# Kernel optimization log

Hardware: AMD Instinct MI355X
Metric: run time of the kernel (lower is better)

Reference implementation:

```python
import jax, jax.numpy as jnp
import numpy as np

NUM_HEADS = 8
CHUNK = 64


def setup_inputs() -> dict:
    key = jax.random.key(0)
    k1, k2, k3, k4 = jax.random.split(key, 4)
    B, C, H, W = 16, 384, 64, 64
    x = jax.random.normal(k1, (B, C, H, W), dtype=jnp.float32)
    # torch nn.Linear weights are [out, in]; qkv has no bias (qkv_bias=False)
    qkv_w = jax.random.normal(k2, (3 * C, C), dtype=jnp.float32) * (C ** -0.5)
    proj_w = jax.random.normal(k3, (C, C), dtype=jnp.float32) * (C ** -0.5)
    proj_b = jax.random.normal(k4, (C,), dtype=jnp.float32) * 0.02
    return {"x": x, "qkv_w": qkv_w, "proj_w": proj_w, "proj_b": proj_b}


def reference(x, qkv_w, proj_w, proj_b):
    B, C, H, W = x.shape
    N = H * W
    nh = NUM_HEADS
    hd = C // nh
    scale = hd ** -0.5
    nc = N // CHUNK  # number of non-overlapping local blocks

    t = x.reshape(B, C, N).transpose(0, 2, 1)  # [B, N, C]
    qkv = t @ qkv_w.T  # [B, N, 3C]
    qkv = qkv.reshape(B, N, 3, nh, hd).transpose(2, 0, 3, 1, 4)  # [3, B, nh, N, hd]
    q, k, v = qkv[0], qkv[1], qkv[2]

    # block-local attention: reshape N -> (nc, CHUNK) and batch over blocks
    q = q.reshape(B, nh, nc, CHUNK, hd)
    k = k.reshape(B, nh, nc, CHUNK, hd)
    v = v.reshape(B, nh, nc, CHUNK, hd)

    scores = jnp.einsum('bhnqd,bhnkd->bhnqk', q, k) * scale  # [B,nh,nc,CHUNK,CHUNK]
    attn = jax.nn.softmax(scores, axis=-1)
    out = jnp.einsum('bhnqk,bhnkd->bhnqd', attn, v)  # [B,nh,nc,CHUNK,hd]

    out = out.reshape(B, nh, N, hd).transpose(0, 2, 1, 3).reshape(B, N, C)
    out = out @ proj_w.T + proj_b
    return out.transpose(0, 2, 1).reshape(B, C, H, W)
```

## Files before the change

### kernel.cpp

```cpp
#include <hip/hip_runtime.h>
#include <stdint.h>

#define NH 8
#define HD 48
#define CC 384
#define NN 4096
#define CK 384

typedef short short8 __attribute__((ext_vector_type(8)));
typedef float floatx4 __attribute__((ext_vector_type(4)));

__device__ inline unsigned short f32_to_bf16_bits(float f) {
    uint32_t u = __builtin_bit_cast(uint32_t, f);
    u = (u + 0x7FFFu + ((u >> 16) & 1u)) >> 16;
    return (unsigned short)u;
}
__device__ inline short8 load8(const unsigned short* p) {
    return *reinterpret_cast<const short8*>(p);
}
typedef __attribute__((address_space(1))) const void gvoid_t;
typedef __attribute__((address_space(3))) void lvoid_t;
__device__ inline void async16(const unsigned short* g, unsigned short* l) {
    __builtin_amdgcn_global_load_lds((gvoid_t*)g, (lvoid_t*)l, 16, 0, 0);
}

__global__ __launch_bounds__(256) void k_cvt(
    const float* __restrict__ src, unsigned short* __restrict__ dst, int n8)
{
    int i = blockIdx.x * 256 + threadIdx.x;
    if (i >= n8) return;
    const float* s = src + (size_t)i * 8;
    unsigned short t[8];
    #pragma unroll
    for (int j = 0; j < 8; ++j) t[j] = f32_to_bf16_bits(s[j]);
    *reinterpret_cast<short8*>(dst + (size_t)i * 8) = *reinterpret_cast<short8*>(t);
}

__global__ __launch_bounds__(256) void k_tr(
    const float* __restrict__ x, unsigned short* __restrict__ xT)
{
    __shared__ unsigned short tile[64][72];
    int bx = blockIdx.x;
    int nt = bx & 63; int rest = bx >> 6; int ct = rest % 6; int b = rest / 6;
    int c0 = ct * 64, n0 = nt * 64;
    int t = threadIdx.x;
    int nl = t & 63, w = t >> 6;
    const float* xb = x + (size_t)b * CC * NN;
    #pragma unroll
    for (int i = 0; i < 4; ++i) {
        int cl = w * 16 + i * 4;
        unsigned short u[4];
        #pragma unroll
        for (int j = 0; j < 4; ++j)
            u[j] = f32_to_bf16_bits(xb[(size_t)(c0 + cl + j) * NN + n0 + nl]);
        *reinterpret_cast<uint2*>(&tile[nl][cl]) = *reinterpret_cast<uint2*>(u);
    }
    __syncthreads();
    #pragma unroll
    for (int it = 0; it < 2; ++it) {
        int v = it * 256 + t;
        int row = v >> 3, seg = v & 7;
        *reinterpret_cast<short8*>(xT + ((size_t)b * NN + n0 + row) * CK + c0 + seg * 8) =
            load8(&tile[row][seg * 8]);
    }
}

__global__ __launch_bounds__(256) void k_qkv(
    const unsigned short* __restrict__ A,
    const unsigned short* __restrict__ W,
    unsigned short* __restrict__ QK,
    unsigned short* __restrict__ Vt)
{
    __shared__ unsigned short smem[17408];
    unsigned short* As = smem;
    unsigned short* Ws = smem + 8192;
    int bx = blockIdx.x;
    int tf = bx % 9, tm = bx / 9;
    int m0 = tm * 128, f0 = tf * 128;
    int tid = threadIdx.x, wid = tid >> 6, lane = tid & 63;
    int l15 = lane & 15, quad = lane >> 4;
    int wm = wid & 1, wn = wid >> 1;

    const unsigned short* Ab = A + (size_t)m0 * CK;
    const unsigned short* Wb = W + (size_t)f0 * CK;

    floatx4 acc[4][4] = {};

    for (int kk = 0; kk < 6; ++kk) {
        int k0 = kk * 64;
        #pragma unroll
        for (int i = 0; i < 4; ++i) {
            int c = i * 256 + tid;
            async16(Ab + (size_t)(c >> 3) * CK + k0 + (c & 7) * 8, As + (i * 256 + wid * 64) * 8);
            async16(Wb + (size_t)(c >> 3) * CK + k0 + (c & 7) * 8, Ws + (i * 256 + wid * 64) * 8);
        }
        __syncthreads();
        #pragma unroll
        for (int ks = 0; ks < 2; ++ks) {
            short8 a[4], bf[4];
            #pragma unroll
            for (int i = 0; i < 4; ++i)
                a[i] = load8(As + (wm * 64 + i * 16 + l15) * 64 + ks * 32 + quad * 8);
            #pragma unroll
            for (int j = 0; j < 4; ++j)
                bf[j] = load8(Ws + (wn * 64 + j * 16 + l15) * 64 + ks * 32 + quad * 8);
            #pragma unroll
            for (int i = 0; i < 4; ++i)
                #pragma unroll
                for (int j = 0; j < 4; ++j)
                    acc[i][j] = __builtin_amdgcn_mfma_f32_16x16x32_bf16(a[i], bf[j], acc[i][j], 0, 0, 0);
        }
        __syncthreads();
    }

    int b = m0 >> 12, nb = m0 & 4095;
    if (tf < 6) {
        #pragma unroll
        for (int i = 0; i < 4; ++i)
            #pragma unroll
            for (int j = 0; j < 4; ++j)
                #pragma unroll
                for (int r = 0; r < 4; ++r)
                    smem[(wm * 64 + i * 16 + quad * 4 + r) * 128 + wn * 64 + j * 16 + l15] =
                        f32_to_bf16_bits(acc[i][j][r]);
        __syncthreads();
        #pragma unroll
        for (int it = 0; it < 8; ++it) {
            int c = it * 256 + tid;
            int row = c >> 4, seg = c & 15;
            *reinterpret_cast<short8*>(QK + (size_t)(m0 + row) * 768 + f0 + seg * 8) =
                load8(smem + row * 128 + seg * 8);
        }
    } else {
        #pragma unroll
        for (int i = 0; i < 4; ++i)
            #pragma unroll
            for (int j = 0; j < 4; ++j)
                #pragma unroll
                for (int r = 0; r < 4; ++r)
                    smem[(wn * 64 + j * 16 + l15) * 136 + wm * 64 + i * 16 + quad * 4 + r] =
                        f32_to_bf16_bits(acc[i][j][r]);
        __syncthreads();
        int fvb = (tf - 6) * 128;
        #pragma unroll
        for (int it = 0; it < 8; ++it) {
            int c = it * 256 + tid;
            int fl = c >> 4, seg = c & 15;
            int fv = fvb + fl;
            int h = fv / 48, d = fv - h * 48;
            *reinterpret_cast<short8*>(Vt + (((size_t)(b * 8 + h) * 48 + d) << 12) + nb + seg * 8) =
                load8(smem + fl * 136 + seg * 8);
        }
    }
}

__global__ __launch_bounds__(256) void k_attn(
    const unsigned short* __restrict__ QK,
    const unsigned short* __restrict__ Vt,
    unsigned short* __restrict__ AO)
{
    __shared__ unsigned short ql[64][64];
    __shared__ unsigned short kl[64][64];
    __shared__ unsigned short vt[48][72];
    __shared__ float          sc[64][66];
    __shared__ unsigned short pl[64][72];

    int bx = blockIdx.x;
    int cn = bx & 63, h = (bx >> 6) & 7, b = bx >> 9;
    int n0 = cn * 64;
    int tid = threadIdx.x, wid = tid >> 6, lane = tid & 63;
    int l15 = lane & 15, quad = lane >> 4;
    int m0w = wid * 16;
    int h48 = h * 48;
    size_t b4 = (size_t)b * NN + n0;

    for (int v = tid; v < 768; v += 256) {
        int mat = v / 384;
        int idx = v - mat * 384;
        int rr = idx / 6, seg = idx - rr * 6;
        uint4 val = *reinterpret_cast<const uint4*>(QK + (b4 + rr) * 768 + mat * 384 + h48 + seg * 8);
        unsigned short* dst = mat ? &kl[rr][seg * 8] : &ql[rr][seg * 8];
        *reinterpret_cast<uint4*>(dst) = val;
    }
    {
        short8 z = {};
        int v = tid;
        if (v < 256) {
            int mat = v >> 7, rr = (v >> 1) & 63, half = v & 1;
            unsigned short* dst = mat ? &kl[rr][48 + half * 8] : &ql[rr][48 + half * 8];
            *reinterpret_cast<short8*>(dst) = z;
        }
    }
    for (int v = tid; v < 384; v += 256) {
        int d = v >> 3, seg = v & 7;
        *reinterpret_cast<uint4*>(&vt[d][seg * 8]) =
            *reinterpret_cast<const uint4*>(Vt + (((size_t)(b * 8 + h) * 48 + d) << 12) + n0 + seg * 8);
    }
    __syncthreads();

    const float scale = 0.14433756729740643f;
    #pragma unroll
    for (int t = 0; t < 4; ++t) {
        floatx4 sacc = {};
        #pragma unroll
        for (int ks = 0; ks < 2; ++ks) {
            short8 a  = load8(&ql[m0w + l15][ks * 32 + quad * 8]);
            short8 bb = load8(&kl[t * 16 + l15][ks * 32 + quad * 8]);
            sacc = __builtin_amdgcn_mfma_f32_16x16x32_bf16(a, bb, sacc, 0, 0, 0);
        }
        #pragma unroll
        for (int r = 0; r < 4; ++r)
            sc[m0w + quad * 4 + r][t * 16 + l15] = sacc[r] * scale;
    }
    __syncthreads();

    {
        int row = m0w + l15;
        int jb  = quad * 16;
        float ev[16];
        #pragma unroll
        for (int jj = 0; jj < 16; ++jj) ev[jj] = sc[row][jb + jj];
        float m = ev[0];
        #pragma unroll
        for (int jj = 1; jj < 16; ++jj) m = fmaxf(m, ev[jj]);
        m = fmaxf(m, __shfl_xor(m, 16));
        m = fmaxf(m, __shfl_xor(m, 32));
        float s = 0.f;
        #pragma unroll
        for (int jj = 0; jj < 16; ++jj) { ev[jj] = __expf(ev[jj] - m); s += ev[jj]; }
        s += __shfl_xor(s, 16);
        s += __shfl_xor(s, 32);
        float inv = 1.0f / s;
        #pragma unroll
        for (int jj = 0; jj < 16; ++jj) pl[row][jb + jj] = f32_to_bf16_bits(ev[jj] * inv);
    }
    __syncthreads();

    #pragma unroll
    for (int t = 0; t < 3; ++t) {
        floatx4 oacc = {};
        #pragma unroll
        for (int ks = 0; ks < 2; ++ks) {
            short8 a  = load8(&pl[m0w + l15][ks * 32 + quad * 8]);
            short8 bb = load8(&vt[t * 16 + l15][ks * 32 + quad * 8]);
            oacc = __builtin_amdgcn_mfma_f32_16x16x32_bf16(a, bb, oacc, 0, 0, 0);
        }
        #pragma unroll
        for (int r = 0; r < 4; ++r)
            kl[m0w + quad * 4 + r][t * 16 + l15] = f32_to_bf16_bits(oacc[r]);
    }
    __syncthreads();

    for (int v = tid; v < 384; v += 256) {
        int rr = v / 6, seg = v - rr * 6;
        *reinterpret_cast<short8*>(AO + (b4 + rr) * CC + h48 + seg * 8) =
            load8(&kl[rr][seg * 8]);
    }
}

__global__ __launch_bounds__(256) void k_proj(
    const unsigned short* __restrict__ A,
    const unsigned short* __restrict__ W,
    const float* __restrict__ bias,
    float* __restrict__ out)
{
    __shared__ unsigned short smem[17408];
    unsigned short* As = smem;
    unsigned short* Ws = smem + 8192;
    float* fs = (float*)smem;
    int bx = blockIdx.x;
    int tf = bx % 3, tm = bx / 3;
    int m0 = tm * 128, f0 = tf * 128;
    int tid = threadIdx.x, wid = tid >> 6, lane = tid & 63;
    int l15 = lane & 15, quad = lane >> 4;
    int wm = wid & 1, wn = wid >> 1;

    const unsigned short* Ab = A + (size_t)m0 * CK;
    const unsigned short* Wb = W + (size_t)f0 * CK;

    floatx4 acc[4][4] = {};

    for (int kk = 0; kk < 6; ++kk) {
        int k0 = kk * 64;
        #pragma unroll
        for (int i = 0; i < 4; ++i) {
            int c = i * 256 + tid;
            async16(Ab + (size_t)(c >> 3) * CK + k0 + (c & 7) * 8, As + (i * 256 + wid * 64) * 8);
            async16(Wb + (size_t)(c >> 3) * CK + k0 + (c & 7) * 8, Ws + (i * 256 + wid * 64) * 8);
        }
        __syncthreads();
        #pragma unroll
        for (int ks = 0; ks < 2; ++ks) {
            short8 a[4], bf[4];
            #pragma unroll
            for (int i = 0; i < 4; ++i)
                a[i] = load8(As + (wm * 64 + i * 16 + l15) * 64 + ks * 32 + quad * 8);
            #pragma unroll
            for (int j = 0; j < 4; ++j)
                bf[j] = load8(Ws + (wn * 64 + j * 16 + l15) * 64 + ks * 32 + quad * 8);
            #pragma unroll
            for (int i = 0; i < 4; ++i)
                #pragma unroll
                for (int j = 0; j < 4; ++j)
                    acc[i][j] = __builtin_amdgcn_mfma_f32_16x16x32_bf16(a[i], bf[j], acc[i][j], 0, 0, 0);
        }
        __syncthreads();
    }

    int b = m0 >> 12, nb = m0 & 4095;
    #pragma unroll
    for (int hh = 0; hh < 2; ++hh) {
        if (wn == hh) {
            #pragma unroll
            for (int j = 0; j < 4; ++j) {
                float bv = bias[f0 + hh * 64 + j * 16 + l15];
                #pragma unroll
                for (int i = 0; i < 4; ++i)
                    #pragma unroll
                    for (int r = 0; r < 4; ++r)
                        fs[(j * 16 + l15) * 132 + wm * 64 + i * 16 + quad * 4 + r] =
                            acc[i][j][r] + bv;
            }
        }
        __syncthreads();
        #pragma unroll
        for (int it = 0; it < 8; ++it) {
            int c = it * 256 + tid;
            int cl = c >> 5, seg = c & 31;
            *reinterpret_cast<float4*>(
                out + (((size_t)(b * CC + f0 + hh * 64 + cl)) << 12) + nb + seg * 4) =
                *reinterpret_cast<const float4*>(fs + cl * 132 + seg * 4);
        }
        __syncthreads();
    }
}

extern "C" void kernel_launch(void* const* d_in, const int* in_sizes, int n_in,
                              void* d_out, int out_size, void* d_ws, size_t ws_size,
                              hipStream_t stream) {
    const float* x      = (const float*)d_in[0];
    const float* qkv_w  = (const float*)d_in[1];
    const float* proj_w = (const float*)d_in[2];
    const float* proj_b = (const float*)d_in[3];
    float* out = (float*)d_out;

    const size_t nX  = (size_t)16 * CC * NN;
    const size_t nW1 = (size_t)3 * CC * CC;
    const size_t nW2 = (size_t)CC * CC;

    unsigned short* xT  = (unsigned short*)d_ws;
    unsigned short* w1b = xT  + nX;
    unsigned short* w2b = w1b + nW1;
    unsigned short* QK  = w2b + nW2;
    unsigned short* Vt  = QK  + (size_t)16 * NN * 768;
    unsigned short* AO  = Vt  + (size_t)16 * 8 * 48 * NN;

    k_tr  <<<dim3(16 * 6 * 64), dim3(256), 0, stream>>>(x, xT);
    k_cvt <<<dim3((int)(nW1 / 8 + 255) / 256), dim3(256), 0, stream>>>(qkv_w, w1b, (int)(nW1 / 8));
    k_cvt <<<dim3((int)(nW2 / 8 + 255) / 256), dim3(256), 0, stream>>>(proj_w, w2b, (int)(nW2 / 8));

    k_qkv <<<dim3(512 * 9), dim3(256), 0, stream>>>(xT, w1b, QK, Vt);
    k_attn<<<dim3(16 * 8 * 64), dim3(256), 0, stream>>>(QK, Vt, AO);
    k_proj<<<dim3(512 * 3), dim3(256), 0, stream>>>(AO, w2b, proj_b, out);
}
```

Measured before the change: 393.1 us.

## Fuse block attention with output projection and remap QKV blocks per XCD

Merges the attention and projection kernels into one kernel per 64-token chunk. The kernel loops over all 8 heads, keeps the attention output for the chunk in LDS, then multiplies it by the projection weights read directly from global memory. This removes the AO round trip through global memory and one launch. The softmax now stays in registers and is redistributed to the PV matmul with shuffles instead of going through LDS. The QKV GEMM block index is also remapped so that consecutive row tiles land on the same XCD for L2 locality. The risks are a large LDS footprint that lowers occupancy, only 1024 blocks, and weights loaded from global without LDS staging.

Measured after the change: 487.2 us. 23.9% more time.

```diff
diff --git a/kernel.cpp b/kernel.cpp
--- a/kernel.cpp
+++ b/kernel.cpp
@@ -75,7 +75,9 @@
     unsigned short* As = smem;
     unsigned short* Ws = smem + 8192;
     int bx = blockIdx.x;
-    int tf = bx % 9, tm = bx / 9;
+    int xcd = bx & 7, idx = bx >> 3;
+    int tm = xcd * 64 + idx / 9;
+    int tf = idx % 9;
     int m0 = tm * 128, f0 = tf * 128;
     int tid = threadIdx.x, wid = tid >> 6, lane = tid & 63;
     int l15 = lane & 15, quad = lane >> 4;
@@ -154,184 +156,145 @@
     }
 }
 
-__global__ __launch_bounds__(256) void k_attn(
+__global__ __launch_bounds__(256) void k_ap(
     const unsigned short* __restrict__ QK,
     const unsigned short* __restrict__ Vt,
-    unsigned short* __restrict__ AO)
+    const unsigned short* __restrict__ W2,
+    const float* __restrict__ bias,
+    float* __restrict__ out)
 {
-    __shared__ unsigned short ql[64][64];
-    __shared__ unsigned short kl[64][64];
+    __shared__ unsigned short kl[64][56];
     __shared__ unsigned short vt[48][72];
-    __shared__ float          sc[64][66];
-    __shared__ unsigned short pl[64][72];
+    __shared__ unsigned short ao[64][392];
 
     int bx = blockIdx.x;
-    int cn = bx & 63, h = (bx >> 6) & 7, b = bx >> 9;
+    int cn = bx & 63, b = bx >> 6;
     int n0 = cn * 64;
     int tid = threadIdx.x, wid = tid >> 6, lane = tid & 63;
     int l15 = lane & 15, quad = lane >> 4;
-    int m0w = wid * 16;
-    int h48 = h * 48;
-    size_t b4 = (size_t)b * NN + n0;
-
-    for (int v = tid; v < 768; v += 256) {
-        int mat = v / 384;
-        int idx = v - mat * 384;
-        int rr = idx / 6, seg = idx - rr * 6;
-        uint4 val = *reinterpret_cast<const uint4*>(QK + (b4 + rr) * 768 + mat * 384 + h48 + seg * 8);
-        unsigned short* dst = mat ? &kl[rr][seg * 8] : &ql[rr][seg * 8];
-        *reinterpret_cast<uint4*>(dst) = val;
-    }
-    {
-        short8 z = {};
-        int v = tid;
-        if (v < 256) {
-            int mat = v >> 7, rr = (v >> 1) & 63, half = v & 1;
-            unsigned short* dst = mat ? &kl[rr][48 + half * 8] : &ql[rr][48 + half * 8];
-            *reinterpret_cast<short8*>(dst) = z;
-        }
-    }
-    for (int v = tid; v < 384; v += 256) {
-        int d = v >> 3, seg = v & 7;
-        *reinterpret_cast<uint4*>(&vt[d][seg * 8]) =
-            *reinterpret_cast<const uint4*>(Vt + (((size_t)(b * 8 + h) * 48 + d) << 12) + n0 + seg * 8);
+    bool hi = quad >= 2;
+    size_t rowbase = (size_t)b * NN + n0;
+
+    const float scale = 0.14433756729740643f;
+    const unsigned short* qrow = QK + (rowbase + wid * 16 + l15) * 768;
+    int d1 = 32 + ((quad & 1) << 3);
+    short8 z8 = {};
+
+    for (int h = 0; h < 8; ++h) {
+        int h48 = h * 48;
+        __syncthreads();
+        for (int v = tid; v < 384; v += 256) {
+            int r = v / 6, sg = v - r * 6;
+            *reinterpret_cast<uint4*>(&kl[r][sg * 8]) =
+                *reinterpret_cast<const uint4*>(QK + (rowbase + r) * 768 + 384 + h48 + sg * 8);
+        }
+        const unsigned short* vbase = Vt + (((size_t)(b * 8 + h) * 48) << 12) + n0;
+        for (int v = tid; v < 384; v += 256) {
+            int d = v >> 3, sg = v & 7;
+            *reinterpret_cast<uint4*>(&vt[d][sg * 8]) =
+                *reinterpret_cast<const uint4*>(vbase + ((size_t)d << 12) + sg * 8);
+        }
+        __syncthreads();
+
+        short8 qf0 = load8(qrow + h48 + quad * 8);
+        short8 qf1 = load8(qrow + h48 + d1);
+        if (hi) qf1 = z8;
+
+        floatx4 st[4];
+        #pragma unroll
+        for (int tk = 0; tk < 4; ++tk) {
+            floatx4 s = {};
+            short8 ka = load8(&kl[tk * 16 + l15][quad * 8]);
+            s = __builtin_amdgcn_mfma_f32_16x16x32_bf16(ka, qf0, s, 0, 0, 0);
+            short8 kb = load8(&kl[tk * 16 + l15][d1]);
+            if (hi) kb = z8;
+            s = __builtin_amdgcn_mfma_f32_16x16x32_bf16(kb, qf1, s, 0, 0, 0);
+            st[tk] = s;
+        }
+
+        float mx = -1e30f;
+        #pragma unroll
+        for (int tk = 0; tk < 4; ++tk)
+            #pragma unroll
+            for (int r = 0; r < 4; ++r) {
+                st[tk][r] *= scale;
+                mx = fmaxf(mx, st[tk][r]);
+            }
+        mx = fmaxf(mx, __shfl_xor(mx, 16));
+        mx = fmaxf(mx, __shfl_xor(mx, 32));
+        float sum = 0.f;
+        #pragma unroll
+        for (int tk = 0; tk < 4; ++tk)
+            #pragma unroll
+            for (int r = 0; r < 4; ++r) {
+                st[tk][r] = __expf(st[tk][r] - mx);
+                sum += st[tk][r];
+            }
+        sum += __shfl_xor(sum, 16);
+        sum += __shfl_xor(sum, 32);
+        float inv = 1.0f / sum;
+        #pragma unroll
+        for (int tk = 0; tk < 4; ++tk)
+            #pragma unroll
+            for (int r = 0; r < 4; ++r)
+                st[tk][r] *= inv;
+
+        int idxA = ((quad & 1) << 5) + l15;
+        int idxB = idxA + 16;
+        short8 pfrag[2];
+        #pragma unroll
+        for (int ks = 0; ks < 2; ++ks) {
+            unsigned short pb[8];
+            #pragma unroll
+            for (int r = 0; r < 4; ++r) {
+                float a0 = __shfl(st[2 * ks + 0][r], idxA);
+                float a1 = __shfl(st[2 * ks + 1][r], idxA);
+                pb[r] = f32_to_bf16_bits(hi ? a1 : a0);
+                float b0 = __shfl(st[2 * ks + 0][r], idxB);
+                float b1 = __shfl(st[2 * ks + 1][r], idxB);
+                pb[4 + r] = f32_to_bf16_bits(hi ? b1 : b0);
+            }
+            pfrag[ks] = *reinterpret_cast<short8*>(pb);
+        }
+
+        #pragma unroll
+        for (int td = 0; td < 3; ++td) {
+            floatx4 o = {};
+            short8 va0 = load8(&vt[td * 16 + l15][quad * 8]);
+            short8 va1 = load8(&vt[td * 16 + l15][32 + quad * 8]);
+            o = __builtin_amdgcn_mfma_f32_16x16x32_bf16(va0, pfrag[0], o, 0, 0, 0);
+            o = __builtin_amdgcn_mfma_f32_16x16x32_bf16(va1, pfrag[1], o, 0, 0, 0);
+            unsigned short ob[4];
+            #pragma unroll
+            for (int r = 0; r < 4; ++r) ob[r] = f32_to_bf16_bits(o[r]);
+            *reinterpret_cast<uint2*>(&ao[wid * 16 + l15][h48 + td * 16 + quad * 4]) =
+                *reinterpret_cast<uint2*>(ob);
+        }
     }
     __syncthreads();
 
-    const float scale = 0.14433756729740643f;
     #pragma unroll
-    for (int t = 0; t < 4; ++t) {
-        floatx4 sacc = {};
-        #pragma unroll
-        for (int ks = 0; ks < 2; ++ks) {
-            short8 a  = load8(&ql[m0w + l15][ks * 32 + quad * 8]);
-            short8 bb = load8(&kl[t * 16 + l15][ks * 32 + quad * 8]);
-            sacc = __builtin_amdgcn_mfma_f32_16x16x32_bf16(a, bb, sacc, 0, 0, 0);
-        }
-        #pragma unroll
-        for (int r = 0; r < 4; ++r)
-            sc[m0w + quad * 4 + r][t * 16 + l15] = sacc[r] * scale;
-    }
-    __syncthreads();
-
-    {
-        int row = m0w + l15;
-        int jb  = quad * 16;
-        float ev[16];
-        #pragma unroll
-        for (int jj = 0; jj < 16; ++jj) ev[jj] = sc[row][jb + jj];
-        float m = ev[0];
-        #pragma unroll
-        for (int jj = 1; jj < 16; ++jj) m = fmaxf(m, ev[jj]);
-        m = fmaxf(m, __shfl_xor(m, 16));
-        m = fmaxf(m, __shfl_xor(m, 32));
-        float s = 0.f;
-        #pragma unroll
-        for (int jj = 0; jj < 16; ++jj) { ev[jj] = __expf(ev[jj] - m); s += ev[jj]; }
-        s += __shfl_xor(s, 16);
-        s += __shfl_xor(s, 32);
-        float inv = 1.0f / s;
-        #pragma unroll
-        for (int jj = 0; jj < 16; ++jj) pl[row][jb + jj] = f32_to_bf16_bits(ev[jj] * inv);
-    }
-    __syncthreads();
-
-    #pragma unroll
-    for (int t = 0; t < 3; ++t) {
-        floatx4 oacc = {};
-        #pragma unroll
-        for (int ks = 0; ks < 2; ++ks) {
-            short8 a  = load8(&pl[m0w + l15][ks * 32 + quad * 8]);
-            short8 bb = load8(&vt[t * 16 + l15][ks * 32 + quad * 8]);
-            oacc = __builtin_amdgcn_mfma_f32_16x16x32_bf16(a, bb, oacc, 0, 0, 0);
-        }
-        #pragma unroll
-        for (int r = 0; r < 4; ++r)
-            kl[m0w + quad * 4 + r][t * 16 + l15] = f32_to_bf16_bits(oacc[r]);
-    }
-    __syncthreads();
-
-    for (int v = tid; v < 384; v += 256) {
-        int rr = v / 6, seg = v - rr * 6;
-        *reinterpret_cast<short8*>(AO + (b4 + rr) * CC + h48 + seg * 8) =
-            load8(&kl[rr][seg * 8]);
-    }
-}
-
-__global__ __launch_bounds__(256) void k_proj(
-    const unsigned short* __restrict__ A,
-    const unsigned short* __restrict__ W,
-    const float* __restrict__ bias,
-    float* __restrict__ out)
-{
-    __shared__ unsigned short smem[17408];
-    unsigned short* As = smem;
-    unsigned short* Ws = smem + 8192;
-    float* fs = (float*)smem;
-    int bx = blockIdx.x;
-    int tf = bx % 3, tm = bx / 3;
-    int m0 = tm * 128, f0 = tf * 128;
-    int tid = threadIdx.x, wid = tid >> 6, lane = tid & 63;
-    int l15 = lane & 15, quad = lane >> 4;
-    int wm = wid & 1, wn = wid >> 1;
-
-    const unsigned short* Ab = A + (size_t)m0 * CK;
-    const unsigned short* Wb = W + (size_t)f0 * CK;
-
-    floatx4 acc[4][4] = {};
-
-    for (int kk = 0; kk < 6; ++kk) {
-        int k0 = kk * 64;
-        #pragma unroll
-        for (int i = 0; i < 4; ++i) {
-            int c = i * 256 + tid;
-            async16(Ab + (size_t)(c >> 3) * CK + k0 + (c & 7) * 8, As + (i * 256 + wid * 64) * 8);
-            async16(Wb + (size_t)(c >> 3) * CK + k0 + (c & 7) * 8, Ws + (i * 256 + wid * 64) * 8);
-        }
-        __syncthreads();
-        #pragma unroll
-        for (int ks = 0; ks < 2; ++ks) {
-            short8 a[4], bf[4];
-            #pragma unroll
-            for (int i = 0; i < 4; ++i)
-                a[i] = load8(As + (wm * 64 + i * 16 + l15) * 64 + ks * 32 + quad * 8);
-            #pragma unroll
-            for (int j = 0; j < 4; ++j)
-                bf[j] = load8(Ws + (wn * 64 + j * 16 + l15) * 64 + ks * 32 + quad * 8);
-            #pragma unroll
-            for (int i = 0; i < 4; ++i)
-                #pragma unroll
-                for (int j = 0; j < 4; ++j)
-                    acc[i][j] = __builtin_amdgcn_mfma_f32_16x16x32_bf16(a[i], bf[j], acc[i][j], 0, 0, 0);
-        }
-        __syncthreads();
-    }
-
-    int b = m0 >> 12, nb = m0 & 4095;
-    #pragma unroll
-    for (int hh = 0; hh < 2; ++hh) {
-        if (wn == hh) {
-            #pragma unroll
-            for (int j = 0; j < 4; ++j) {
-                float bv = bias[f0 + hh * 64 + j * 16 + l15];
-                #pragma unroll
-                for (int i = 0; i < 4; ++i)
-                    #pragma unroll
-                    for (int r = 0; r < 4; ++r)
-                        fs[(j * 16 + l15) * 132 + wm * 64 + i * 16 + quad * 4 + r] =
-                            acc[i][j][r] + bv;
+    for (int half = 0; half < 2; ++half) {
+        floatx4 acc[12] = {};
+        #pragma unroll
+        for (int s = 0; s < 12; ++s) {
+            short8 a = load8(&ao[wid * 16 + l15][s * 32 + quad * 8]);
+            #pragma unroll
+            for (int nt = 0; nt < 12; ++nt) {
+                short8 bf = load8(W2 + (size_t)(half * 192 + nt * 16 + l15) * 384 + s * 32 + quad * 8);
+                acc[nt] = __builtin_amdgcn_mfma_f32_16x16x32_bf16(a, bf, acc[nt], 0, 0, 0);
             }
         }
-        __syncthreads();
-        #pragma unroll
-        for (int it = 0; it < 8; ++it) {
-            int c = it * 256 + tid;
-            int cl = c >> 5, seg = c & 31;
+        #pragma unroll
+        for (int nt = 0; nt < 12; ++nt) {
+            int cout = half * 192 + nt * 16 + l15;
+            float bv = bias[cout];
+            float4 v;
+            v.x = acc[nt][0] + bv; v.y = acc[nt][1] + bv;
+            v.z = acc[nt][2] + bv; v.w = acc[nt][3] + bv;
             *reinterpret_cast<float4*>(
-                out + (((size_t)(b * CC + f0 + hh * 64 + cl)) << 12) + nb + seg * 4) =
-                *reinterpret_cast<const float4*>(fs + cl * 132 + seg * 4);
-        }
-        __syncthreads();
+                out + (((size_t)(b * CC + cout)) << 12) + n0 + wid * 16 + quad * 4) = v;
+        }
     }
 }
 
@@ -353,13 +316,11 @@
     unsigned short* w2b = w1b + nW1;
     unsigned short* QK  = w2b + nW2;
     unsigned short* Vt  = QK  + (size_t)16 * NN * 768;
-    unsigned short* AO  = Vt  + (size_t)16 * 8 * 48 * NN;
 
     k_tr  <<<dim3(16 * 6 * 64), dim3(256), 0, stream>>>(x, xT);
     k_cvt <<<dim3((int)(nW1 / 8 + 255) / 256), dim3(256), 0, stream>>>(qkv_w, w1b, (int)(nW1 / 8));
     k_cvt <<<dim3((int)(nW2 / 8 + 255) / 256), dim3(256), 0, stream>>>(proj_w, w2b, (int)(nW2 / 8));
 
-    k_qkv <<<dim3(512 * 9), dim3(256), 0, stream>>>(xT, w1b, QK, Vt);
-    k_attn<<<dim3(16 * 8 * 64), dim3(256), 0, stream>>>(QK, Vt, AO);
-    k_proj<<<dim3(512 * 3), dim3(256), 0, stream>>>(AO, w2b, proj_b, out);
-}
+    k_qkv <<<dim3(4608), dim3(256), 0, stream>>>(xT, w1b, QK, Vt);
+    k_ap  <<<dim3(1024), dim3(256), 0, stream>>>(QK, Vt, w2b, proj_b, out);
+}
```
